# Performance work log

Hardware: AMD Instinct MI355X
Metric: run time of the kernel (lower is better)

The kernel has to match this reference:

```python
import jax, jax.numpy as jnp
import numpy as np

IN_FEATURES = 4096
OUT_FEATURES = 4096
NUM_CLUSTERS = 65536
CLUSTER_DIM = 4
DEFICIENCY = (CLUSTER_DIM - OUT_FEATURES % CLUSTER_DIM) % CLUSTER_DIM  # 0 here
INDEX_LEN = IN_FEATURES * (OUT_FEATURES + DEFICIENCY) // CLUSTER_DIM


def setup_inputs() -> dict:
    key = jax.random.key(0)
    k_x, k_c, k_i, k_b = jax.random.split(key, 4)
    x = jax.random.normal(k_x, (4, 2048, IN_FEATURES), dtype=jnp.float32)
    cluster = jax.random.normal(k_c, (NUM_CLUSTERS, CLUSTER_DIM), dtype=jnp.float32)
    index = jax.random.randint(k_i, (INDEX_LEN,), 0, NUM_CLUSTERS, dtype=jnp.int32)
    bias = jax.random.normal(k_b, (OUT_FEATURES,), dtype=jnp.float32)
    return {"x": x, "cluster": cluster, "index": index, "bias": bias}


def reference(x, cluster, index, bias):
    # Gather codebook vectors and reassemble the weight matrix [in, out(+pad)]
    vectors = cluster[index]                              # [INDEX_LEN, CLUSTER_DIM]
    weight = vectors.reshape(IN_FEATURES, -1)             # [in, out + deficiency]
    if DEFICIENCY > 0:
        weight = weight[:, :-DEFICIENCY]                  # crop padding columns
    # x: [B, S, in] @ weight: [in, out] -> [B, S, out]
    out = jnp.matmul(x, weight) + bias
    return out
```

## Files before the change

### kernel.cpp

```cpp
#include <hip/hip_runtime.h>
#include <hip/hip_bf16.h>
#include <stdint.h>

typedef unsigned short u16;
typedef __attribute__((ext_vector_type(8))) short bf16x8;
typedef __attribute__((ext_vector_type(4))) float f32x4;

#define KD 4096
#define ND 4096
#define MD 8192
#define NKT 64

__device__ __forceinline__ u16 f2bf(float f) {
    uint32_t u = __float_as_uint(f);
    u += 0x7FFFu + ((u >> 16) & 1u);
    return (u16)(u >> 16);
}

__device__ __forceinline__ void gload_lds16(const u16* g, u16* l) {
    __builtin_amdgcn_global_load_lds(
        (const __attribute__((address_space(1))) void*)g,
        (__attribute__((address_space(3))) void*)l, 16, 0, 0);
}

__global__ __launch_bounds__(256) void build_wt(
    const int* __restrict__ index, const float4* __restrict__ cluster4,
    u16* __restrict__ wt) {
    __shared__ int idx_s[64][32];
    const int t  = threadIdx.x;
    const int k0 = blockIdx.x * 64;
    const int g0 = blockIdx.y * 32;
    #pragma unroll
    for (int r = 0; r < 8; ++r) {
        int k = (t >> 5) + r * 8;
        int g = t & 31;
        idx_s[k][g] = index[(size_t)(k0 + k) * 1024 + g0 + g];
    }
    __syncthreads();
    const int g_local = t >> 3;
    const int k_local = (t & 7) * 8;
    u16 pk[4][8];
    #pragma unroll
    for (int j = 0; j < 8; ++j) {
        int idx = idx_s[k_local + j][g_local];
        float4 v = cluster4[idx];
        pk[0][j] = f2bf(v.x);
        pk[1][j] = f2bf(v.y);
        pk[2][j] = f2bf(v.z);
        pk[3][j] = f2bf(v.w);
    }
    const size_t nbase = (size_t)g0 * 4 + g_local * 4;
    #pragma unroll
    for (int c = 0; c < 4; ++c) {
        *reinterpret_cast<uint4*>(wt + (nbase + c) * KD + k0 + k_local) =
            *reinterpret_cast<const uint4*>(pk[c]);
    }
}

__global__ __launch_bounds__(256) void cvt_x(
    const float4* __restrict__ x4, uint4* __restrict__ xb) {
    int i = blockIdx.x * 256 + threadIdx.x;
    float4 a = x4[2 * i];
    float4 b = x4[2 * i + 1];
    u16 r[8] = {f2bf(a.x), f2bf(a.y), f2bf(a.z), f2bf(a.w),
                f2bf(b.x), f2bf(b.y), f2bf(b.z), f2bf(b.w)};
    xb[i] = *reinterpret_cast<const uint4*>(r);
}

__global__ __launch_bounds__(512, 2) void gemm256(
    const u16* __restrict__ A,
    const u16* __restrict__ Bt,
    const float* __restrict__ bias,
    float* __restrict__ C) {
    __shared__ __align__(16) u16 lds[65536];

    const int t    = threadIdx.x;
    const int lane = t & 63;
    const int wave = t >> 6;
    const int wm   = wave >> 2;
    const int wn   = wave & 3;

    const int bid = blockIdx.x;
    const int swz = (bid & 7) * 64 + (bid >> 3);
    const int n0  = (swz & 15) * 256;
    const int m0  = (swz >> 4) * 256;

    const u16* srcA[2]; const u16* srcB[2];
    #pragma unroll
    for (int i = 0; i < 2; ++i) {
        int p   = i * 8192 + t * 16;
        int row = p >> 7;
        int cb  = (p & 127) ^ ((row & 7) << 4);
        srcA[i] = A  + (size_t)(m0 + row) * KD + (cb >> 1);
        srcB[i] = Bt + (size_t)(n0 + row) * KD + (cb >> 1);
    }
    const size_t HS = (size_t)128 * KD;

    const int frow = lane & 15;
    int ce2[2];
    #pragma unroll
    for (int s = 0; s < 2; ++s)
        ce2[s] = ((s * 64 + ((lane >> 4) * 16)) ^ ((lane & 7) << 4)) >> 1;

    f32x4 acc[8][4] = {};
    bf16x8 aS[2][4][2];
    bf16x8 bR[2][2];

#define STAGE(isB, b, h, kt) do {                                          \
    _Pragma("unroll")                                                      \
    for (int i_ = 0; i_ < 2; ++i_) {                                       \
        const u16* s_ = ((isB) ? srcB[i_] : srcA[i_])                      \
                        + (size_t)(h) * HS + (kt) * 64;                    \
        u16* d_ = (u16*)lds + (b) * 32768 + (isB) * 16384                  \
                  + (h) * 8192 + i_ * 4096 + t * 8;                        \
        gload_lds16(s_, d_);                                               \
    } } while (0)

#define READA(b, mh) do {                                                  \
    _Pragma("unroll") for (int f_ = 0; f_ < 4; ++f_)                       \
    _Pragma("unroll") for (int s_ = 0; s_ < 2; ++s_)                       \
        aS[mh][f_][s_] = *(const bf16x8*)((u16*)lds + (b) * 32768 +        \
            ((wm * 128 + (mh) * 64 + f_ * 16 + frow) * 64) + ce2[s_]);     \
    } while (0)

#define READB(b, nh) do {                                                  \
    _Pragma("unroll") for (int g_ = 0; g_ < 2; ++g_)                       \
    _Pragma("unroll") for (int s_ = 0; s_ < 2; ++s_)                       \
        bR[g_][s_] = *(const bf16x8*)((u16*)lds + (b) * 32768 + 16384 +    \
            ((wn * 64 + (nh) * 32 + g_ * 16 + frow) * 64) + ce2[s_]);      \
    } while (0)

#define MFMA16(mh, nh) do {                                                \
    _Pragma("unroll") for (int f_ = 0; f_ < 4; ++f_)                       \
    _Pragma("unroll") for (int g_ = 0; g_ < 2; ++g_)                       \
    _Pragma("unroll") for (int s_ = 0; s_ < 2; ++s_)                       \
        acc[(mh)*4+f_][(nh)*2+g_] = __builtin_amdgcn_mfma_f32_16x16x32_bf16( \
            aS[mh][f_][s_], bR[g_][s_], acc[(mh)*4+f_][(nh)*2+g_], 0,0,0); \
    } while (0)

#define BAR() __builtin_amdgcn_s_barrier()
#define WAIT_LGKM() do { asm volatile("s_waitcnt lgkmcnt(0)" ::: "memory"); \
                         __builtin_amdgcn_sched_barrier(0); } while (0)
#define WAIT_VM4() asm volatile("s_waitcnt vmcnt(4)" ::: "memory")

    STAGE(0, 0, 0, 0);
    STAGE(0, 0, 1, 0);
    STAGE(1, 0, 0, 0);
    STAGE(1, 0, 1, 0);
    STAGE(1, 1, 0, 1);
    STAGE(0, 1, 0, 1);
    WAIT_VM4();
    BAR();

    for (int I = 0; I < NKT / 2; ++I) {
        const int tb  = 2 * I + 1;
        const int tp2 = (2 * I + 2) & (NKT - 1);
        const int tp3 = (2 * I + 3) & (NKT - 1);

        READA(0, 0); READB(0, 0); STAGE(0, 1, 1, tb);
        BAR(); WAIT_LGKM();
        __builtin_amdgcn_s_setprio(1); MFMA16(0, 0); __builtin_amdgcn_s_setprio(0);
        BAR();
        READA(0, 1); STAGE(1, 1, 1, tb);
        BAR(); WAIT_LGKM();
        __builtin_amdgcn_s_setprio(1); MFMA16(1, 0); __builtin_amdgcn_s_setprio(0);
        BAR();
        READB(0, 1); STAGE(1, 0, 0, tp2);
        BAR(); WAIT_LGKM();
        __builtin_amdgcn_s_setprio(1); MFMA16(0, 1); __builtin_amdgcn_s_setprio(0);
        BAR();
        STAGE(0, 0, 0, tp2);
        BAR(); WAIT_LGKM();
        __builtin_amdgcn_s_setprio(1); MFMA16(1, 1); __builtin_amdgcn_s_setprio(0);
        WAIT_VM4();
        BAR();
        READA(1, 0); READB(1, 0); STAGE(0, 0, 1, tp2);
        BAR(); WAIT_LGKM();
        __builtin_amdgcn_s_setprio(1); MFMA16(0, 0); __builtin_amdgcn_s_setprio(0);
        BAR();
        READA(1, 1); STAGE(1, 0, 1, tp2);
        BAR(); WAIT_LGKM();
        __builtin_amdgcn_s_setprio(1); MFMA16(1, 0); __builtin_amdgcn_s_setprio(0);
        BAR();
        READB(1, 1); STAGE(1, 1, 0, tp3);
        BAR(); WAIT_LGKM();
        __builtin_amdgcn_s_setprio(1); MFMA16(0, 1); __builtin_amdgcn_s_setprio(0);
        BAR();
        STAGE(0, 1, 0, tp3);
        BAR(); WAIT_LGKM();
        __builtin_amdgcn_s_setprio(1); MFMA16(1, 1); __builtin_amdgcn_s_setprio(0);
        WAIT_VM4();
        BAR();
    }

    const int crow = (lane >> 4) * 4;
    float bv[4];
    #pragma unroll
    for (int g = 0; g < 4; ++g)
        bv[g] = bias[n0 + wn * 64 + g * 16 + frow];
    #pragma unroll
    for (int f = 0; f < 8; ++f) {
        const int mrow = m0 + wm * 128 + f * 16 + crow;
        #pragma unroll
        for (int g = 0; g < 4; ++g) {
            float* cp = C + (size_t)mrow * ND + n0 + wn * 64 + g * 16 + frow;
            #pragma unroll
            for (int r = 0; r < 4; ++r)
                cp[(size_t)r * ND] = acc[f][g][r] + bv[g];
        }
    }
#undef STAGE
#undef READA
#undef READB
#undef MFMA16
#undef BAR
#undef WAIT_LGKM
#undef WAIT_VM4
}

__global__ __launch_bounds__(256) void fallback_gemm(
    const float* __restrict__ x, const float4* __restrict__ cluster4,
    const int* __restrict__ index, const float* __restrict__ bias,
    float* __restrict__ out) {
    const int m = blockIdx.y;
    const int g = blockIdx.x * 256 + threadIdx.x;
    const float* xr = x + (size_t)m * KD;
    float a0 = 0.f, a1 = 0.f, a2 = 0.f, a3 = 0.f;
    for (int k = 0; k < KD; ++k) {
        float xv = xr[k];
        float4 cv = cluster4[index[(size_t)k * 1024 + g]];
        a0 += xv * cv.x; a1 += xv * cv.y; a2 += xv * cv.z; a3 += xv * cv.w;
    }
    size_t o = (size_t)m * ND + (size_t)g * 4;
    out[o + 0] = a0 + bias[g * 4 + 0];
    out[o + 1] = a1 + bias[g * 4 + 1];
    out[o + 2] = a2 + bias[g * 4 + 2];
    out[o + 3] = a3 + bias[g * 4 + 3];
}

extern "C" void kernel_launch(void* const* d_in, const int* in_sizes, int n_in,
                              void* d_out, int out_size, void* d_ws, size_t ws_size,
                              hipStream_t stream) {
    const float* x       = (const float*)d_in[0];
    const float* cluster = (const float*)d_in[1];
    const int*   index   = (const int*)d_in[2];
    const float* bias    = (const float*)d_in[3];
    float* out = (float*)d_out;

    const size_t WT_BYTES = (size_t)ND * KD * sizeof(u16);
    const size_t XB_BYTES = (size_t)MD * KD * sizeof(u16);

    if (ws_size >= WT_BYTES + XB_BYTES) {
        u16* wt = (u16*)d_ws;
        u16* xb = (u16*)((char*)d_ws + WT_BYTES);
        build_wt<<<dim3(KD / 64, ND / 128), 256, 0, stream>>>(
            index, (const float4*)cluster, wt);
        cvt_x<<<(MD * KD / 8) / 256, 256, 0, stream>>>(
            (const float4*)x, (uint4*)xb);
        gemm256<<<dim3((MD / 256) * (ND / 256)), 512, 0, stream>>>(
            xb, wt, bias, out);
    } else {
        fallback_gemm<<<dim3(1024 / 256, MD), 256, 0, stream>>>(
            x, (const float4*)cluster, index, bias, out);
    }
}
```

Baseline: 276.3 us.

## Double-buffer LDS fragment registers to overlap LDS reads with MFMA

Adds a second register stage for the A and B fragments so LDS reads for the next quadrant are issued before the current MFMA block runs. Waits become partial lgkmcnt counts instead of full drains, so ds_reads overlap with matrix math. The last quadrant's fragments are prefetched across the loop boundary, and an extra prologue read is added. The cost is more VGPRs (roughly double the fragment registers), which could reduce occupancy or cause spills, plus more delicate waitcnt accounting.

```diff
diff --git a/kernel.cpp b/kernel.cpp
--- a/kernel.cpp
+++ b/kernel.cpp
@@ -104,7 +104,7 @@
 
     f32x4 acc[8][4] = {};
     bf16x8 aS[2][4][2];
-    bf16x8 bR[2][2];
+    bf16x8 bS[2][2][2];
 
 #define STAGE(isB, b, h, kt) do {                                          \
     _Pragma("unroll")                                                      \
@@ -116,32 +116,36 @@
         gload_lds16(s_, d_);                                               \
     } } while (0)
 
-#define READA(b, mh) do {                                                  \
+#define READA(st, b, mh) do {                                              \
     _Pragma("unroll") for (int f_ = 0; f_ < 4; ++f_)                       \
     _Pragma("unroll") for (int s_ = 0; s_ < 2; ++s_)                       \
-        aS[mh][f_][s_] = *(const bf16x8*)((u16*)lds + (b) * 32768 +        \
+        aS[st][f_][s_] = *(const bf16x8*)((u16*)lds + (b) * 32768 +        \
             ((wm * 128 + (mh) * 64 + f_ * 16 + frow) * 64) + ce2[s_]);     \
     } while (0)
 
-#define READB(b, nh) do {                                                  \
+#define READB(st, b, nh) do {                                              \
     _Pragma("unroll") for (int g_ = 0; g_ < 2; ++g_)                       \
     _Pragma("unroll") for (int s_ = 0; s_ < 2; ++s_)                       \
-        bR[g_][s_] = *(const bf16x8*)((u16*)lds + (b) * 32768 + 16384 +    \
+        bS[st][g_][s_] = *(const bf16x8*)((u16*)lds + (b) * 32768 + 16384 +\
             ((wn * 64 + (nh) * 32 + g_ * 16 + frow) * 64) + ce2[s_]);      \
     } while (0)
 
-#define MFMA16(mh, nh) do {                                                \
+#define MFMAQ(ast, bst, mh, nh) do {                                       \
     _Pragma("unroll") for (int f_ = 0; f_ < 4; ++f_)                       \
     _Pragma("unroll") for (int g_ = 0; g_ < 2; ++g_)                       \
     _Pragma("unroll") for (int s_ = 0; s_ < 2; ++s_)                       \
         acc[(mh)*4+f_][(nh)*2+g_] = __builtin_amdgcn_mfma_f32_16x16x32_bf16( \
-            aS[mh][f_][s_], bR[g_][s_], acc[(mh)*4+f_][(nh)*2+g_], 0,0,0); \
+            aS[ast][f_][s_], bS[bst][g_][s_], acc[(mh)*4+f_][(nh)*2+g_],   \
+            0, 0, 0);                                                      \
     } while (0)
 
-#define BAR() __builtin_amdgcn_s_barrier()
-#define WAIT_LGKM() do { asm volatile("s_waitcnt lgkmcnt(0)" ::: "memory"); \
-                         __builtin_amdgcn_sched_barrier(0); } while (0)
-#define WAIT_VM4() asm volatile("s_waitcnt vmcnt(4)" ::: "memory")
+#define BAR()  __builtin_amdgcn_s_barrier()
+#define SB()   __builtin_amdgcn_sched_barrier(0)
+#define WLG(N) do { asm volatile("s_waitcnt lgkmcnt(" #N ")" ::: "memory"); \
+                    __builtin_amdgcn_sched_barrier(0); } while (0)
+#define WVM(N) asm volatile("s_waitcnt vmcnt(" #N ")" ::: "memory")
+#define PRIO1() __builtin_amdgcn_s_setprio(1)
+#define PRIO0() __builtin_amdgcn_s_setprio(0)
 
     STAGE(0, 0, 0, 0);
     STAGE(0, 0, 1, 0);
@@ -149,48 +153,45 @@
     STAGE(1, 0, 1, 0);
     STAGE(1, 1, 0, 1);
     STAGE(0, 1, 0, 1);
-    WAIT_VM4();
+    WVM(4);
     BAR();
+    READA(0, 0, 0);
+    READB(0, 0, 0);
+    SB();
 
     for (int I = 0; I < NKT / 2; ++I) {
         const int tb  = 2 * I + 1;
         const int tp2 = (2 * I + 2) & (NKT - 1);
         const int tp3 = (2 * I + 3) & (NKT - 1);
 
-        READA(0, 0); READB(0, 0); STAGE(0, 1, 1, tb);
-        BAR(); WAIT_LGKM();
-        __builtin_amdgcn_s_setprio(1); MFMA16(0, 0); __builtin_amdgcn_s_setprio(0);
+        READB(1, 0, 1); STAGE(0, 1, 1, tb); SB();
+        BAR(); WLG(4);
+        PRIO1(); MFMAQ(0, 0, 0, 0); PRIO0(); BAR();
+        READA(1, 0, 1); STAGE(1, 1, 1, tb); SB();
+        BAR(); WLG(8);
+        PRIO1(); MFMAQ(0, 1, 0, 1); PRIO0(); BAR();
+        STAGE(1, 0, 0, tp2); SB();
+        BAR(); WLG(0);
+        PRIO1(); MFMAQ(1, 0, 1, 0); PRIO0(); BAR();
+        STAGE(0, 0, 0, tp2);
+        WVM(4);
         BAR();
-        READA(0, 1); STAGE(1, 1, 1, tb);
-        BAR(); WAIT_LGKM();
-        __builtin_amdgcn_s_setprio(1); MFMA16(1, 0); __builtin_amdgcn_s_setprio(0);
+        READA(0, 1, 0); READB(0, 1, 0); SB();
+        PRIO1(); MFMAQ(1, 1, 1, 1); PRIO0(); BAR();
+        READB(1, 1, 1); STAGE(0, 0, 1, tp2); SB();
+        BAR(); WLG(4);
+        PRIO1(); MFMAQ(0, 0, 0, 0); PRIO0(); BAR();
+        READA(1, 1, 1); STAGE(1, 0, 1, tp2); SB();
+        BAR(); WLG(8);
+        PRIO1(); MFMAQ(0, 1, 0, 1); PRIO0(); BAR();
+        STAGE(1, 1, 0, tp3); SB();
+        BAR(); WLG(0);
+        PRIO1(); MFMAQ(1, 0, 1, 0); PRIO0(); BAR();
+        STAGE(0, 1, 0, tp3);
+        WVM(4);
         BAR();
-        READB(0, 1); STAGE(1, 0, 0, tp2);
-        BAR(); WAIT_LGKM();
-        __builtin_amdgcn_s_setprio(1); MFMA16(0, 1); __builtin_amdgcn_s_setprio(0);
-        BAR();
-        STAGE(0, 0, 0, tp2);
-        BAR(); WAIT_LGKM();
-        __builtin_amdgcn_s_setprio(1); MFMA16(1, 1); __builtin_amdgcn_s_setprio(0);
-        WAIT_VM4();
-        BAR();
-        READA(1, 0); READB(1, 0); STAGE(0, 0, 1, tp2);
-        BAR(); WAIT_LGKM();
-        __builtin_amdgcn_s_setprio(1); MFMA16(0, 0); __builtin_amdgcn_s_setprio(0);
-        BAR();
-        READA(1, 1); STAGE(1, 0, 1, tp2);
-        BAR(); WAIT_LGKM();
-        __builtin_amdgcn_s_setprio(1); MFMA16(1, 0); __builtin_amdgcn_s_setprio(0);
-        BAR();
-        READB(1, 1); STAGE(1, 1, 0, tp3);
-        BAR(); WAIT_LGKM();
-        __builtin_amdgcn_s_setprio(1); MFMA16(0, 1); __builtin_amdgcn_s_setprio(0);
-        BAR();
-        STAGE(0, 1, 0, tp3);
-        BAR(); WAIT_LGKM();
-        __builtin_amdgcn_s_setprio(1); MFMA16(1, 1); __builtin_amdgcn_s_setprio(0);
-        WAIT_VM4();
-        BAR();
+        READA(0, 0, 0); READB(0, 0, 0); SB();
+        PRIO1(); MFMAQ(1, 1, 1, 1); PRIO0(); BAR();
     }
 
     const int crow = (lane >> 4) * 4;
@@ -212,10 +213,11 @@
 #undef STAGE
 #undef READA
 #undef READB
-#undef MFMA16
+#undef MFMAQ
 #undef BAR
-#undef WAIT_LGKM
-#undef WAIT_VM4
+#undef SB
+#undef WLG
+#undef WVM
 }
 
 __global__ __launch_bounds__(256) void fallback_gemm(
```

New measurement: 381.0 us. +37.9%, slower.
